# Kernel optimization log

Measured on AMD Instinct MI355X. Metric: run time of the kernel, lower is better.

Reference implementation:

```python
import jax, jax.numpy as jnp
import numpy as np

N = 50000
IN_DIM = 1024
HID = 64
HEADS = 4
OUT_DIM = 128
NEG_SLOPE = 0.2


def setup_inputs() -> dict:
    key = jax.random.key(0)
    ks = jax.random.split(key, 10)
    x = jax.random.normal(ks[0], (N, IN_DIM), dtype=jnp.float32)
    edge_index = jax.random.randint(ks[1], (2, 800000), 0, N, dtype=jnp.int64)
    # GATConv 1: input_dim -> hidden_dim, heads=HEADS, concat=True
    W1 = jax.random.normal(ks[2], (IN_DIM, HEADS * HID), dtype=jnp.float32) * (1.0 / np.sqrt(IN_DIM))
    att_src1 = jax.random.normal(ks[3], (HEADS, HID), dtype=jnp.float32) * 0.1
    att_dst1 = jax.random.normal(ks[4], (HEADS, HID), dtype=jnp.float32) * 0.1
    b1 = jnp.zeros((HEADS * HID,), dtype=jnp.float32)
    # GATConv 2: hidden_dim*heads -> output_dim, heads=1, concat=False
    W2 = jax.random.normal(ks[5], (HEADS * HID, OUT_DIM), dtype=jnp.float32) * (1.0 / np.sqrt(HEADS * HID))
    att_src2 = jax.random.normal(ks[6], (1, OUT_DIM), dtype=jnp.float32) * 0.1
    att_dst2 = jax.random.normal(ks[7], (1, OUT_DIM), dtype=jnp.float32) * 0.1
    b2 = jnp.zeros((OUT_DIM,), dtype=jnp.float32)
    return {"x": x, "edge_index": edge_index, "W1": W1, "att_src1": att_src1,
            "att_dst1": att_dst1, "b1": b1, "W2": W2, "att_src2": att_src2,
            "att_dst2": att_dst2, "b2": b2}


def _gat_conv(x, src, dst, W, a_src, a_dst, b, heads, concat):
    # x: [N, F_in]; src/dst: [E'] (self-loops already included)
    n = x.shape[0]
    h = (x @ W).reshape(n, heads, -1)                 # [N, H, D]
    # per-node attention halves (PyG style)
    alpha_s = jnp.sum(h * a_src[None], axis=-1)       # [N, H]
    alpha_d = jnp.sum(h * a_dst[None], axis=-1)       # [N, H]
    e = jax.nn.leaky_relu(alpha_s[src] + alpha_d[dst], NEG_SLOPE)  # [E', H]
    # segment softmax over incoming edges of each destination node
    m = jax.ops.segment_max(e, dst, num_segments=n)   # [N, H]
    m = jnp.where(jnp.isfinite(m), m, 0.0)
    e = jnp.exp(e - m[dst])
    s = jax.ops.segment_sum(e, dst, num_segments=n)   # [N, H]
    alpha = e / (s[dst] + 1e-16)                      # [E', H]
    out = jax.ops.segment_sum(h[src] * alpha[:, :, None], dst, num_segments=n)  # [N, H, D]
    out = out.reshape(n, -1) if concat else out.mean(axis=1)
    return out + b


def reference(x, edge_index, W1, att_src1, att_dst1, b1, W2, att_src2, att_dst2, b2):
    n = x.shape[0]
    # PyG GATConv default: add self-loops
    loops = jnp.arange(n, dtype=edge_index.dtype)
    src = jnp.concatenate([edge_index[0], loops])
    dst = jnp.concatenate([edge_index[1], loops])
    # dropout layers are identity in eval mode
    h = _gat_conv(x, src, dst, W1, att_src1, att_dst1, b1, HEADS, concat=True)
    h = jax.nn.elu(h)
    out = _gat_conv(h, src, dst, W2, att_src2, att_dst2, b2, 1, concat=False)
    # F.normalize(p=2, dim=-1)
    norm = jnp.maximum(jnp.linalg.norm(out, axis=-1, keepdims=True), 1e-12)
    return out / norm
```

## Files before the change

### kernel.cpp

```cpp
#include <hip/hip_runtime.h>
#include <math.h>

#define NNODES 50000
#define E0 800000
#define ETOT 850000
#define IN_DIM 1024
#define HEADS 4
#define C1 256
#define C2 128
#define NEG_SLOPE 0.2f

typedef short bf16x8 __attribute__((ext_vector_type(8)));
typedef float f32x4 __attribute__((ext_vector_type(4)));
typedef unsigned short ushort_t;

__device__ __forceinline__ void edge_sd(const int* __restrict__ ei, int e, int& s, int& d) {
    if (e < E0) { s = ei[e]; d = ei[E0 + e]; }
    else        { s = e - E0; d = s; }
}

__device__ __forceinline__ ushort_t f2b(float f) {
    unsigned u = __float_as_uint(f);
    return (ushort_t)((u + 0x7fffu + ((u >> 16) & 1u)) >> 16);
}
__device__ __forceinline__ float bf2f(ushort_t u) {
    return __uint_as_float((unsigned)u << 16);
}
__device__ __forceinline__ float lrelu(float v) { return v > 0.f ? v : NEG_SLOPE * v; }

__device__ __forceinline__ void gload_lds16(const void* g, void* l) {
    __builtin_amdgcn_global_load_lds(
        (const __attribute__((address_space(1))) unsigned int*)g,
        (__attribute__((address_space(3))) unsigned int*)l, 16, 0, 0);
}

__global__ __launch_bounds__(256) void wtrans_kernel(const float* __restrict__ W,
                                                     ushort_t* __restrict__ WT,
                                                     int K, int N)
{
    int idx = blockIdx.x * 256 + threadIdx.x;
    if (idx >= K * N) return;
    int k = idx / N, n = idx % N;
    WT[(size_t)n * K + k] = f2b(W[idx]);
}

__global__ __launch_bounds__(256, 3) void gemm_fb(const float* __restrict__ A,
                                                  const ushort_t* __restrict__ Bt,
                                                  ushort_t* __restrict__ Cb,
                                                  int M, int N, int K)
{
    __shared__ __align__(16) ushort_t As[2][4 * 128 * 8];
    __shared__ __align__(16) ushort_t Bs[2][4 * 128 * 8];

    const int tid  = threadIdx.x;
    const int lane = tid & 63;
    const int wid  = tid >> 6;
    const int wr   = wid >> 1, wc = wid & 1;
    const int rowBase = blockIdx.y * 128;
    const int colBase = blockIdx.x * 128;

    const int arow = tid >> 1;
    const int akh  = (tid & 1) * 2;
    const int aGRow = min(rowBase + arow, M - 1);
    const float* aptr = A + (size_t)aGRow * K + akh * 8;
    const int awoff0 = akh * 1024 + arow * 8;
    const int awoff1 = awoff0 + 1024;

    const ushort_t* bptr = Bt + (size_t)(colBase + lane) * K + wid * 8;
    const int bwoff0 = wid * 1024;
    const int bwoff1 = bwoff0 + 512;

    const int r0 = lane & 15;
    const int kh = lane >> 4;
    const int ardoff = kh * 1024 + (wr * 64 + r0) * 8;
    const int brdoff = kh * 1024 + (wc * 64 + r0) * 8;

    f32x4 zero = {0.f, 0.f, 0.f, 0.f};
    f32x4 acc[4][4];
    #pragma unroll
    for (int i = 0; i < 4; ++i)
        #pragma unroll
        for (int j = 0; j < 4; ++j) acc[i][j] = zero;

    {
        float4 f0 = *(const float4*)(aptr + 0);
        float4 f1 = *(const float4*)(aptr + 4);
        float4 f2 = *(const float4*)(aptr + 8);
        float4 f3 = *(const float4*)(aptr + 12);
        bf16x8 p0, p1;
        p0[0] = f2b(f0.x); p0[1] = f2b(f0.y); p0[2] = f2b(f0.z); p0[3] = f2b(f0.w);
        p0[4] = f2b(f1.x); p0[5] = f2b(f1.y); p0[6] = f2b(f1.z); p0[7] = f2b(f1.w);
        p1[0] = f2b(f2.x); p1[1] = f2b(f2.y); p1[2] = f2b(f2.z); p1[3] = f2b(f2.w);
        p1[4] = f2b(f3.x); p1[5] = f2b(f3.y); p1[6] = f2b(f3.z); p1[7] = f2b(f3.w);
        *(bf16x8*)&As[0][awoff0] = p0;
        *(bf16x8*)&As[0][awoff1] = p1;
        gload_lds16(bptr, &Bs[0][bwoff0]);
        gload_lds16(bptr + (size_t)64 * K, &Bs[0][bwoff1]);
    }
    __syncthreads();

    const ushort_t* rdA = As[0]; const ushort_t* rdB = Bs[0];
    ushort_t*       stA = As[1]; ushort_t*       stB = Bs[1];

    const int nt = K >> 5;
    for (int t = 0; t < nt; ++t) {
        const int kt = (t + 1) << 5;
        const bool has_next = kt < K;
        float4 f0, f1, f2, f3;
        if (has_next) {
            gload_lds16(bptr + kt, stB + bwoff0);
            gload_lds16(bptr + (size_t)64 * K + kt, stB + bwoff1);
            f0 = *(const float4*)(aptr + kt + 0);
            f1 = *(const float4*)(aptr + kt + 4);
            f2 = *(const float4*)(aptr + kt + 8);
            f3 = *(const float4*)(aptr + kt + 12);
        }

        bf16x8 af[4], bfr[4];
        #pragma unroll
        for (int fi = 0; fi < 4; ++fi) af[fi] = *(const bf16x8*)(rdA + ardoff + fi * 128);
        #pragma unroll
        for (int fj = 0; fj < 4; ++fj) bfr[fj] = *(const bf16x8*)(rdB + brdoff + fj * 128);
        #pragma unroll
        for (int fi = 0; fi < 4; ++fi)
            #pragma unroll
            for (int fj = 0; fj < 4; ++fj)
                acc[fi][fj] = __builtin_amdgcn_mfma_f32_16x16x32_bf16(
                    af[fi], bfr[fj], acc[fi][fj], 0, 0, 0);

        if (has_next) {
            bf16x8 p0, p1;
            p0[0] = f2b(f0.x); p0[1] = f2b(f0.y); p0[2] = f2b(f0.z); p0[3] = f2b(f0.w);
            p0[4] = f2b(f1.x); p0[5] = f2b(f1.y); p0[6] = f2b(f1.z); p0[7] = f2b(f1.w);
            p1[0] = f2b(f2.x); p1[1] = f2b(f2.y); p1[2] = f2b(f2.z); p1[3] = f2b(f2.w);
            p1[4] = f2b(f3.x); p1[5] = f2b(f3.y); p1[6] = f2b(f3.z); p1[7] = f2b(f3.w);
            *(bf16x8*)(stA + awoff0) = p0;
            *(bf16x8*)(stA + awoff1) = p1;
        }
        __syncthreads();
        const ushort_t* tA = rdA; rdA = stA; stA = (ushort_t*)tA;
        const ushort_t* tB = rdB; rdB = stB; stB = (ushort_t*)tB;
    }

    #pragma unroll
    for (int fi = 0; fi < 4; ++fi) {
        int row0 = rowBase + wr * 64 + fi * 16 + kh * 4;
        #pragma unroll
        for (int i = 0; i < 4; ++i) {
            int row = row0 + i;
            if (row < M) {
                #pragma unroll
                for (int fj = 0; fj < 4; ++fj)
                    Cb[(size_t)row * N + colBase + wc * 64 + fj * 16 + r0] = f2b(acc[fi][fj][i]);
            }
        }
    }
}

__global__ __launch_bounds__(256, 4) void gemm_bb(const ushort_t* __restrict__ Ab,
                                                  const ushort_t* __restrict__ Bt,
                                                  ushort_t* __restrict__ Cb,
                                                  int M, int N, int K)
{
    __shared__ __align__(16) ushort_t As[2][4 * 128 * 8];
    __shared__ __align__(16) ushort_t Bs[2][4 * 128 * 8];

    const int tid  = threadIdx.x;
    const int lane = tid & 63;
    const int wid  = tid >> 6;
    const int wr   = wid >> 1, wc = wid & 1;
    const int rowBase = blockIdx.y * 128;
    const int colBase = blockIdx.x * 128;

    const ushort_t* aptr0 = Ab + (size_t)min(rowBase + lane, M - 1) * K + wid * 8;
    const ushort_t* aptr1 = Ab + (size_t)min(rowBase + 64 + lane, M - 1) * K + wid * 8;
    const ushort_t* bptr  = Bt + (size_t)(colBase + lane) * K + wid * 8;
    const int woff0 = wid * 1024;
    const int woff1 = woff0 + 512;

    const int r0 = lane & 15;
    const int kh = lane >> 4;
    const int ardoff = kh * 1024 + (wr * 64 + r0) * 8;
    const int brdoff = kh * 1024 + (wc * 64 + r0) * 8;

    f32x4 zero = {0.f, 0.f, 0.f, 0.f};
    f32x4 acc[4][4];
    #pragma unroll
    for (int i = 0; i < 4; ++i)
        #pragma unroll
        for (int j = 0; j < 4; ++j) acc[i][j] = zero;

    gload_lds16(aptr0, &As[0][woff0]);
    gload_lds16(aptr1, &As[0][woff1]);
    gload_lds16(bptr,  &Bs[0][woff0]);
    gload_lds16(bptr + (size_t)64 * K, &Bs[0][woff1]);
    __syncthreads();

    const ushort_t* rdA = As[0]; const ushort_t* rdB = Bs[0];
    ushort_t*       stA = As[1]; ushort_t*       stB = Bs[1];

    const int nt = K >> 5;
    for (int t = 0; t < nt; ++t) {
        const int kt = (t + 1) << 5;
        if (kt < K) {
            gload_lds16(aptr0 + kt, stA + woff0);
            gload_lds16(aptr1 + kt, stA + woff1);
            gload_lds16(bptr + kt,  stB + woff0);
            gload_lds16(bptr + (size_t)64 * K + kt, stB + woff1);
        }

        bf16x8 af[4], bfr[4];
        #pragma unroll
        for (int fi = 0; fi < 4; ++fi) af[fi] = *(const bf16x8*)(rdA + ardoff + fi * 128);
        #pragma unroll
        for (int fj = 0; fj < 4; ++fj) bfr[fj] = *(const bf16x8*)(rdB + brdoff + fj * 128);
        #pragma unroll
        for (int fi = 0; fi < 4; ++fi)
            #pragma unroll
            for (int fj = 0; fj < 4; ++fj)
                acc[fi][fj] = __builtin_amdgcn_mfma_f32_16x16x32_bf16(
                    af[fi], bfr[fj], acc[fi][fj], 0, 0, 0);

        __syncthreads();
        const ushort_t* tA = rdA; rdA = stA; stA = (ushort_t*)tA;
        const ushort_t* tB = rdB; rdB = stB; stB = (ushort_t*)tB;
    }

    #pragma unroll
    for (int fi = 0; fi < 4; ++fi) {
        int row0 = rowBase + wr * 64 + fi * 16 + kh * 4;
        #pragma unroll
        for (int i = 0; i < 4; ++i) {
            int row = row0 + i;
            if (row < M) {
                #pragma unroll
                for (int fj = 0; fj < 4; ++fj)
                    Cb[(size_t)row * N + colBase + wc * 64 + fj * 16 + r0] = f2b(acc[fi][fj][i]);
            }
        }
    }
}

__global__ __launch_bounds__(256) void alpha1_kernel(const ushort_t* __restrict__ h1b,
                                                     const float* __restrict__ asrc,
                                                     const float* __restrict__ adst,
                                                     float* __restrict__ out_s,
                                                     float* __restrict__ out_d)
{
    int n = blockIdx.x;
    int t = threadIdx.x;
    float h = bf2f(h1b[(size_t)n * C1 + t]);
    float s = h * asrc[t];
    float d = h * adst[t];
    #pragma unroll
    for (int off = 32; off > 0; off >>= 1) {
        s += __shfl_down(s, off);
        d += __shfl_down(d, off);
    }
    if ((t & 63) == 0) {
        out_s[n * HEADS + (t >> 6)] = s;
        out_d[n * HEADS + (t >> 6)] = d;
    }
}

__global__ __launch_bounds__(64) void alpha2_kernel(const ushort_t* __restrict__ h2b,
                                                    const float* __restrict__ asrc,
                                                    const float* __restrict__ adst,
                                                    float* __restrict__ out_s,
                                                    float* __restrict__ out_d)
{
    int n = blockIdx.x;
    int t = threadIdx.x;
    float a = bf2f(h2b[(size_t)n * C2 + t]);
    float b = bf2f(h2b[(size_t)n * C2 + t + 64]);
    float s = a * asrc[t] + b * asrc[t + 64];
    float d = a * adst[t] + b * adst[t + 64];
    #pragma unroll
    for (int off = 32; off > 0; off >>= 1) {
        s += __shfl_down(s, off);
        d += __shfl_down(d, off);
    }
    if (t == 0) { out_s[n] = s; out_d[n] = d; }
}

__global__ __launch_bounds__(256) void deg_kernel(const int* __restrict__ ei,
                                                  int* __restrict__ deg)
{
    int e = blockIdx.x * blockDim.x + threadIdx.x;
    if (e >= ETOT) return;
    int s, d; edge_sd(ei, e, s, d);
    atomicAdd(&deg[d], 1);
}

#define SCAN_T 1024
__global__ __launch_bounds__(SCAN_T) void scan_kernel(const int* __restrict__ deg,
                                                      int* __restrict__ rowptr)
{
    __shared__ int wsum[16];
    __shared__ int chunk_tot;
    __shared__ int carry_s;
    const int t = threadIdx.x, lane = t & 63, w = t >> 6;
    if (t == 0) carry_s = 0;
    __syncthreads();
    for (int base = 0; base < NNODES; base += SCAN_T * 4) {
        int idx = base + t * 4;
        int v0 = (idx + 0 < NNODES) ? deg[idx + 0] : 0;
        int v1 = (idx + 1 < NNODES) ? deg[idx + 1] : 0;
        int v2 = (idx + 2 < NNODES) ? deg[idx + 2] : 0;
        int v3 = (idx + 3 < NNODES) ? deg[idx + 3] : 0;
        int p0 = v0, p1 = p0 + v1, p2 = p1 + v2, p3 = p2 + v3;
        int incl = p3;
        #pragma unroll
        for (int off = 1; off < 64; off <<= 1) {
            int nb = __shfl_up(incl, off);
            if (lane >= off) incl += nb;
        }
        if (lane == 63) wsum[w] = incl;
        __syncthreads();
        if (w == 0 && lane < 16) {
            int ws = wsum[lane];
            int wincl = ws;
            #pragma unroll
            for (int off = 1; off < 16; off <<= 1) {
                int nb = __shfl_up(wincl, off);
                if (lane >= off) wincl += nb;
            }
            wsum[lane] = wincl - ws;
            if (lane == 15) chunk_tot = wincl;
        }
        __syncthreads();
        int carry = carry_s;
        int basev = carry + wsum[w] + (incl - p3);
        if (idx + 0 < NNODES) rowptr[idx + 0] = basev;
        if (idx + 1 < NNODES) rowptr[idx + 1] = basev + p0;
        if (idx + 2 < NNODES) rowptr[idx + 2] = basev + p1;
        if (idx + 3 < NNODES) rowptr[idx + 3] = basev + p2;
        __syncthreads();
        if (t == 0) carry_s = carry + chunk_tot;
        __syncthreads();
    }
    if (threadIdx.x == 0) rowptr[NNODES] = carry_s;
}

__global__ __launch_bounds__(256) void scatter_kernel(const int* __restrict__ ei,
                                                      int* __restrict__ cursor,
                                                      int* __restrict__ srcs)
{
    int e = blockIdx.x * blockDim.x + threadIdx.x;
    if (e >= ETOT) return;
    int s, d; edge_sd(ei, e, s, d);
    int pos = atomicAdd(&cursor[d], 1);
    srcs[pos] = s;
}

__global__ __launch_bounds__(256) void weights1_kernel(const int* __restrict__ rowptr,
                                                       const int* __restrict__ srcs,
                                                       const float4* __restrict__ as1,
                                                       const float4* __restrict__ ad1,
                                                       float4* __restrict__ wbuf)
{
    int d = blockIdx.x * 4 + (threadIdx.x >> 6);
    if (d >= NNODES) return;
    int lane = threadIdx.x & 63;
    int beg = rowptr[d], end = rowptr[d + 1];
    float4 adv = ad1[d];
    float m0 = -INFINITY, m1 = -INFINITY, m2 = -INFINITY, m3 = -INFINITY;
    for (int i = beg + lane; i < end; i += 64) {
        int s = srcs[i];
        float4 av = as1[s];
        m0 = fmaxf(m0, lrelu(av.x + adv.x));
        m1 = fmaxf(m1, lrelu(av.y + adv.y));
        m2 = fmaxf(m2, lrelu(av.z + adv.z));
        m3 = fmaxf(m3, lrelu(av.w + adv.w));
    }
    #pragma unroll
    for (int off = 32; off > 0; off >>= 1) {
        m0 = fmaxf(m0, __shfl_xor(m0, off));
        m1 = fmaxf(m1, __shfl_xor(m1, off));
        m2 = fmaxf(m2, __shfl_xor(m2, off));
        m3 = fmaxf(m3, __shfl_xor(m3, off));
    }
    float s0 = 0.f, s1 = 0.f, s2 = 0.f, s3 = 0.f;
    for (int i = beg + lane; i < end; i += 64) {
        int s = srcs[i];
        float4 av = as1[s];
        float w0 = expf(lrelu(av.x + adv.x) - m0);
        float w1 = expf(lrelu(av.y + adv.y) - m1);
        float w2 = expf(lrelu(av.z + adv.z) - m2);
        float w3 = expf(lrelu(av.w + adv.w) - m3);
        wbuf[i] = make_float4(w0, w1, w2, w3);
        s0 += w0; s1 += w1; s2 += w2; s3 += w3;
    }
    #pragma unroll
    for (int off = 32; off > 0; off >>= 1) {
        s0 += __shfl_xor(s0, off);
        s1 += __shfl_xor(s1, off);
        s2 += __shfl_xor(s2, off);
        s3 += __shfl_xor(s3, off);
    }
    float i0 = 1.f / (s0 + 1e-16f), i1 = 1.f / (s1 + 1e-16f);
    float i2 = 1.f / (s2 + 1e-16f), i3 = 1.f / (s3 + 1e-16f);
    for (int i = beg + lane; i < end; i += 64) {
        float4 wv = wbuf[i];
        wbuf[i] = make_float4(wv.x * i0, wv.y * i1, wv.z * i2, wv.w * i3);
    }
}

__global__ __launch_bounds__(256) void weights2_kernel(const int* __restrict__ rowptr,
                                                       const int* __restrict__ srcs,
                                                       const float* __restrict__ as2,
                                                       const float* __restrict__ ad2,
                                                       float* __restrict__ wbuf)
{
    int d = blockIdx.x * 4 + (threadIdx.x >> 6);
    if (d >= NNODES) return;
    int lane = threadIdx.x & 63;
    int beg = rowptr[d], end = rowptr[d + 1];
    float adv = ad2[d];
    float m = -INFINITY;
    for (int i = beg + lane; i < end; i += 64)
        m = fmaxf(m, lrelu(as2[srcs[i]] + adv));
    #pragma unroll
    for (int off = 32; off > 0; off >>= 1) m = fmaxf(m, __shfl_xor(m, off));
    float sm = 0.f;
    for (int i = beg + lane; i < end; i += 64) {
        float w = expf(lrelu(as2[srcs[i]] + adv) - m);
        wbuf[i] = w;
        sm += w;
    }
    #pragma unroll
    for (int off = 32; off > 0; off >>= 1) sm += __shfl_xor(sm, off);
    float inv = 1.f / (sm + 1e-16f);
    for (int i = beg + lane; i < end; i += 64) wbuf[i] *= inv;
}

__global__ __launch_bounds__(256) void aggr1_csr(const int* __restrict__ rowptr,
                                                 const int* __restrict__ srcs,
                                                 const ushort_t* __restrict__ h1b,
                                                 const float* __restrict__ wbuf,
                                                 const float* __restrict__ b1,
                                                 ushort_t* __restrict__ out)
{
    int d = blockIdx.x;
    int t = threadIdx.x;
    int head = t >> 6;
    int beg = rowptr[d], end = rowptr[d + 1];
    float acc = 0.f;
    int i = beg;
    for (; i + 1 < end; i += 2) {
        int s0 = srcs[i], s1 = srcs[i + 1];
        float a0 = wbuf[i * 4 + head], a1 = wbuf[i * 4 + 4 + head];
        float v0 = bf2f(h1b[(size_t)s0 * C1 + t]);
        float v1 = bf2f(h1b[(size_t)s1 * C1 + t]);
        acc = fmaf(a0, v0, acc);
        acc = fmaf(a1, v1, acc);
    }
    if (i < end) {
        int s0 = srcs[i];
        acc = fmaf(wbuf[i * 4 + head], bf2f(h1b[(size_t)s0 * C1 + t]), acc);
    }
    float o = acc + b1[t];
    out[(size_t)d * C1 + t] = f2b(o > 0.f ? o : (expf(o) - 1.f));
}

__global__ __launch_bounds__(128) void aggr2_csr(const int* __restrict__ rowptr,
                                                 const int* __restrict__ srcs,
                                                 const ushort_t* __restrict__ h2b,
                                                 const float* __restrict__ wbuf,
                                                 const float* __restrict__ b2,
                                                 float* __restrict__ out)
{
    int d = blockIdx.x;
    int t = threadIdx.x;
    int beg = rowptr[d], end = rowptr[d + 1];
    float acc = 0.f;
    int i = beg;
    for (; i + 1 < end; i += 2) {
        int s0 = srcs[i], s1 = srcs[i + 1];
        float a0 = wbuf[i], a1 = wbuf[i + 1];
        float v0 = bf2f(h2b[(size_t)s0 * C2 + t]);
        float v1 = bf2f(h2b[(size_t)s1 * C2 + t]);
        acc = fmaf(a0, v0, acc);
        acc = fmaf(a1, v1, acc);
    }
    if (i < end) acc = fmaf(wbuf[i], bf2f(h2b[(size_t)srcs[i] * C2 + t]), acc);
    float o = acc + b2[t];
    __shared__ float red[2];
    float sq = o * o;
    #pragma unroll
    for (int off = 32; off > 0; off >>= 1) sq += __shfl_down(sq, off);
    if ((t & 63) == 0) red[t >> 6] = sq;
    __syncthreads();
    float total = red[0] + red[1];
    float inv = 1.0f / fmaxf(sqrtf(total), 1e-12f);
    out[(size_t)d * C2 + t] = o * inv;
}

extern "C" void kernel_launch(void* const* d_in, const int* in_sizes, int n_in,
                              void* d_out, int out_size, void* d_ws, size_t ws_size,
                              hipStream_t stream)
{
    const float* x     = (const float*)d_in[0];
    const int*   ei    = (const int*)d_in[1];
    const float* W1    = (const float*)d_in[2];
    const float* asrc1 = (const float*)d_in[3];
    const float* adst1 = (const float*)d_in[4];
    const float* b1    = (const float*)d_in[5];
    const float* W2    = (const float*)d_in[6];
    const float* asrc2 = (const float*)d_in[7];
    const float* adst2 = (const float*)d_in[8];
    const float* b2    = (const float*)d_in[9];
    float* out = (float*)d_out;

    char* ws = (char*)d_ws;
    size_t off = 0;
    auto alloc = [&](size_t nbytes) {
        void* p = ws + off;
        off += (nbytes + 15) & ~(size_t)15;
        return p;
    };
    ushort_t* h1b    = (ushort_t*)alloc((size_t)NNODES * C1 * 2);
    ushort_t* act1b  = (ushort_t*)alloc((size_t)NNODES * C1 * 2);
    ushort_t* h2b    = (ushort_t*)alloc((size_t)NNODES * C2 * 2);
    ushort_t* W1T    = (ushort_t*)alloc((size_t)C1 * IN_DIM * 2);
    ushort_t* W2T    = (ushort_t*)alloc((size_t)C2 * C1 * 2);
    float*    as1    = (float*)alloc((size_t)NNODES * HEADS * 4);
    float*    ad1    = (float*)alloc((size_t)NNODES * HEADS * 4);
    float*    as2    = (float*)alloc((size_t)NNODES * 4);
    float*    ad2    = (float*)alloc((size_t)NNODES * 4);
    float*    wbuf1  = (float*)alloc((size_t)ETOT * HEADS * 4);
    float*    wbuf2  = (float*)alloc((size_t)ETOT * 4);
    int*      deg    = (int*)alloc((size_t)NNODES * 4);
    int*      rowptr = (int*)alloc((size_t)(NNODES + 1) * 4);
    int*      cursor = (int*)alloc((size_t)(NNODES + 1) * 4);
    int*      srcs   = (int*)alloc((size_t)ETOT * 4);

    const int eb = (ETOT + 255) / 256;
    const int nb4 = (NNODES + 3) / 4;

    wtrans_kernel<<<(IN_DIM * C1 + 255) / 256, 256, 0, stream>>>(W1, W1T, IN_DIM, C1);
    wtrans_kernel<<<(C1 * C2 + 255) / 256, 256, 0, stream>>>(W2, W2T, C1, C2);

    hipMemsetAsync(deg, 0, (size_t)NNODES * 4, stream);
    deg_kernel<<<eb, 256, 0, stream>>>(ei, deg);
    scan_kernel<<<1, SCAN_T, 0, stream>>>(deg, rowptr);
    hipMemcpyAsync(cursor, rowptr, (size_t)(NNODES + 1) * 4, hipMemcpyDeviceToDevice, stream);
    scatter_kernel<<<eb, 256, 0, stream>>>(ei, cursor, srcs);

    dim3 g1(C1 / 128, (NNODES + 127) / 128);
    gemm_fb<<<g1, 256, 0, stream>>>(x, W1T, h1b, NNODES, C1, IN_DIM);
    alpha1_kernel<<<NNODES, 256, 0, stream>>>(h1b, asrc1, adst1, as1, ad1);
    weights1_kernel<<<nb4, 256, 0, stream>>>(rowptr, srcs, (const float4*)as1,
                                             (const float4*)ad1, (float4*)wbuf1);
    aggr1_csr<<<NNODES, 256, 0, stream>>>(rowptr, srcs, h1b, wbuf1, b1, act1b);

    dim3 g2(C2 / 128, (NNODES + 127) / 128);
    gemm_bb<<<g2, 256, 0, stream>>>(act1b, W2T, h2b, NNODES, C2, C1);
    alpha2_kernel<<<NNODES, 64, 0, stream>>>(h2b, asrc2, adst2, as2, ad2);
    weights2_kernel<<<nb4, 256, 0, stream>>>(rowptr, srcs, as2, ad2, wbuf2);
    aggr2_csr<<<NNODES, 128, 0, stream>>>(rowptr, srcs, h2b, wbuf2, b2, out);
}
```

Before: 539.5 us.

## Halve GEMM row tiles and aggregate one node per wavefront with vector loads

Both GEMMs change from 128x128 to 64x128 tiles, with a smaller A staging buffer and half the accumulators, and their occupancy hint rises to 6 blocks per CU. The aim is more blocks and more waves in flight for the tall-skinny GEMMs, at the cost of re-reading the B tile more often. The two aggregation kernels now give each node one 64-lane wavefront instead of a whole block, with vectorized bf16 gathers (4 or 2 channels per lane). The layer-2 L2 norm becomes a wave-level xor shuffle reduction, which removes the LDS exchange and __syncthreads.

```diff
diff --git a/kernel.cpp b/kernel.cpp
--- a/kernel.cpp
+++ b/kernel.cpp
@@ -44,27 +44,26 @@
     WT[(size_t)n * K + k] = f2b(W[idx]);
 }
 
-__global__ __launch_bounds__(256, 3) void gemm_fb(const float* __restrict__ A,
+__global__ __launch_bounds__(256, 6) void gemm_fb(const float* __restrict__ A,
                                                   const ushort_t* __restrict__ Bt,
                                                   ushort_t* __restrict__ Cb,
                                                   int M, int N, int K)
 {
-    __shared__ __align__(16) ushort_t As[2][4 * 128 * 8];
+    __shared__ __align__(16) ushort_t As[2][4 * 64 * 8];
     __shared__ __align__(16) ushort_t Bs[2][4 * 128 * 8];
 
     const int tid  = threadIdx.x;
     const int lane = tid & 63;
     const int wid  = tid >> 6;
     const int wr   = wid >> 1, wc = wid & 1;
-    const int rowBase = blockIdx.y * 128;
+    const int rowBase = blockIdx.y * 64;
     const int colBase = blockIdx.x * 128;
 
-    const int arow = tid >> 1;
-    const int akh  = (tid & 1) * 2;
+    const int arow = tid >> 2;
+    const int akc  = tid & 3;
     const int aGRow = min(rowBase + arow, M - 1);
-    const float* aptr = A + (size_t)aGRow * K + akh * 8;
-    const int awoff0 = akh * 1024 + arow * 8;
-    const int awoff1 = awoff0 + 1024;
+    const float* aptr = A + (size_t)aGRow * K + akc * 8;
+    const int awoff = akc * 512 + arow * 8;
 
     const ushort_t* bptr = Bt + (size_t)(colBase + lane) * K + wid * 8;
     const int bwoff0 = wid * 1024;
@@ -72,28 +71,23 @@
 
     const int r0 = lane & 15;
     const int kh = lane >> 4;
-    const int ardoff = kh * 1024 + (wr * 64 + r0) * 8;
+    const int ardoff = kh * 512 + (wr * 32 + r0) * 8;
     const int brdoff = kh * 1024 + (wc * 64 + r0) * 8;
 
     f32x4 zero = {0.f, 0.f, 0.f, 0.f};
-    f32x4 acc[4][4];
-    #pragma unroll
-    for (int i = 0; i < 4; ++i)
+    f32x4 acc[2][4];
+    #pragma unroll
+    for (int i = 0; i < 2; ++i)
         #pragma unroll
         for (int j = 0; j < 4; ++j) acc[i][j] = zero;
 
     {
         float4 f0 = *(const float4*)(aptr + 0);
         float4 f1 = *(const float4*)(aptr + 4);
-        float4 f2 = *(const float4*)(aptr + 8);
-        float4 f3 = *(const float4*)(aptr + 12);
-        bf16x8 p0, p1;
+        bf16x8 p0;
         p0[0] = f2b(f0.x); p0[1] = f2b(f0.y); p0[2] = f2b(f0.z); p0[3] = f2b(f0.w);
         p0[4] = f2b(f1.x); p0[5] = f2b(f1.y); p0[6] = f2b(f1.z); p0[7] = f2b(f1.w);
-        p1[0] = f2b(f2.x); p1[1] = f2b(f2.y); p1[2] = f2b(f2.z); p1[3] = f2b(f2.w);
-        p1[4] = f2b(f3.x); p1[5] = f2b(f3.y); p1[6] = f2b(f3.z); p1[7] = f2b(f3.w);
-        *(bf16x8*)&As[0][awoff0] = p0;
-        *(bf16x8*)&As[0][awoff1] = p1;
+        *(bf16x8*)&As[0][awoff] = p0;
         gload_lds16(bptr, &Bs[0][bwoff0]);
         gload_lds16(bptr + (size_t)64 * K, &Bs[0][bwoff1]);
     }
@@ -106,36 +100,31 @@
     for (int t = 0; t < nt; ++t) {
         const int kt = (t + 1) << 5;
         const bool has_next = kt < K;
-        float4 f0, f1, f2, f3;
+        float4 f0, f1;
         if (has_next) {
             gload_lds16(bptr + kt, stB + bwoff0);
             gload_lds16(bptr + (size_t)64 * K + kt, stB + bwoff1);
             f0 = *(const float4*)(aptr + kt + 0);
             f1 = *(const float4*)(aptr + kt + 4);
-            f2 = *(const float4*)(aptr + kt + 8);
-            f3 = *(const float4*)(aptr + kt + 12);
-        }
-
-        bf16x8 af[4], bfr[4];
-        #pragma unroll
-        for (int fi = 0; fi < 4; ++fi) af[fi] = *(const bf16x8*)(rdA + ardoff + fi * 128);
+        }
+
+        bf16x8 af[2], bfr[4];
+        #pragma unroll
+        for (int fi = 0; fi < 2; ++fi) af[fi] = *(const bf16x8*)(rdA + ardoff + fi * 128);
         #pragma unroll
         for (int fj = 0; fj < 4; ++fj) bfr[fj] = *(const bf16x8*)(rdB + brdoff + fj * 128);
         #pragma unroll
-        for (int fi = 0; fi < 4; ++fi)
+        for (int fi = 0; fi < 2; ++fi)
             #pragma unroll
             for (int fj = 0; fj < 4; ++fj)
                 acc[fi][fj] = __builtin_amdgcn_mfma_f32_16x16x32_bf16(
                     af[fi], bfr[fj], acc[fi][fj], 0, 0, 0);
 
         if (has_next) {
-            bf16x8 p0, p1;
+            bf16x8 p0;
             p0[0] = f2b(f0.x); p0[1] = f2b(f0.y); p0[2] = f2b(f0.z); p0[3] = f2b(f0.w);
             p0[4] = f2b(f1.x); p0[5] = f2b(f1.y); p0[6] = f2b(f1.z); p0[7] = f2b(f1.w);
-            p1[0] = f2b(f2.x); p1[1] = f2b(f2.y); p1[2] = f2b(f2.z); p1[3] = f2b(f2.w);
-            p1[4] = f2b(f3.x); p1[5] = f2b(f3.y); p1[6] = f2b(f3.z); p1[7] = f2b(f3.w);
-            *(bf16x8*)(stA + awoff0) = p0;
-            *(bf16x8*)(stA + awoff1) = p1;
+            *(bf16x8*)(stA + awoff) = p0;
         }
         __syncthreads();
         const ushort_t* tA = rdA; rdA = stA; stA = (ushort_t*)tA;
@@ -143,8 +132,8 @@
     }
 
     #pragma unroll
-    for (int fi = 0; fi < 4; ++fi) {
-        int row0 = rowBase + wr * 64 + fi * 16 + kh * 4;
+    for (int fi = 0; fi < 2; ++fi) {
+        int row0 = rowBase + wr * 32 + fi * 16 + kh * 4;
         #pragma unroll
         for (int i = 0; i < 4; ++i) {
             int row = row0 + i;
@@ -157,43 +146,42 @@
     }
 }
 
-__global__ __launch_bounds__(256, 4) void gemm_bb(const ushort_t* __restrict__ Ab,
+__global__ __launch_bounds__(256, 6) void gemm_bb(const ushort_t* __restrict__ Ab,
                                                   const ushort_t* __restrict__ Bt,
                                                   ushort_t* __restrict__ Cb,
                                                   int M, int N, int K)
 {
-    __shared__ __align__(16) ushort_t As[2][4 * 128 * 8];
+    __shared__ __align__(16) ushort_t As[2][4 * 64 * 8];
     __shared__ __align__(16) ushort_t Bs[2][4 * 128 * 8];
 
     const int tid  = threadIdx.x;
     const int lane = tid & 63;
     const int wid  = tid >> 6;
     const int wr   = wid >> 1, wc = wid & 1;
-    const int rowBase = blockIdx.y * 128;
+    const int rowBase = blockIdx.y * 64;
     const int colBase = blockIdx.x * 128;
 
-    const ushort_t* aptr0 = Ab + (size_t)min(rowBase + lane, M - 1) * K + wid * 8;
-    const ushort_t* aptr1 = Ab + (size_t)min(rowBase + 64 + lane, M - 1) * K + wid * 8;
-    const ushort_t* bptr  = Bt + (size_t)(colBase + lane) * K + wid * 8;
-    const int woff0 = wid * 1024;
-    const int woff1 = woff0 + 512;
+    const ushort_t* aptr = Ab + (size_t)min(rowBase + lane, M - 1) * K + wid * 8;
+    const ushort_t* bptr = Bt + (size_t)(colBase + lane) * K + wid * 8;
+    const int awoff  = wid * 512;
+    const int bwoff0 = wid * 1024;
+    const int bwoff1 = bwoff0 + 512;
 
     const int r0 = lane & 15;
     const int kh = lane >> 4;
-    const int ardoff = kh * 1024 + (wr * 64 + r0) * 8;
+    const int ardoff = kh * 512 + (wr * 32 + r0) * 8;
     const int brdoff = kh * 1024 + (wc * 64 + r0) * 8;
 
     f32x4 zero = {0.f, 0.f, 0.f, 0.f};
-    f32x4 acc[4][4];
-    #pragma unroll
-    for (int i = 0; i < 4; ++i)
+    f32x4 acc[2][4];
+    #pragma unroll
+    for (int i = 0; i < 2; ++i)
         #pragma unroll
         for (int j = 0; j < 4; ++j) acc[i][j] = zero;
 
-    gload_lds16(aptr0, &As[0][woff0]);
-    gload_lds16(aptr1, &As[0][woff1]);
-    gload_lds16(bptr,  &Bs[0][woff0]);
-    gload_lds16(bptr + (size_t)64 * K, &Bs[0][woff1]);
+    gload_lds16(aptr, &As[0][awoff]);
+    gload_lds16(bptr, &Bs[0][bwoff0]);
+    gload_lds16(bptr + (size_t)64 * K, &Bs[0][bwoff1]);
     __syncthreads();
 
     const ushort_t* rdA = As[0]; const ushort_t* rdB = Bs[0];
@@ -203,19 +191,18 @@
     for (int t = 0; t < nt; ++t) {
         const int kt = (t + 1) << 5;
         if (kt < K) {
-            gload_lds16(aptr0 + kt, stA + woff0);
-            gload_lds16(aptr1 + kt, stA + woff1);
-            gload_lds16(bptr + kt,  stB + woff0);
-            gload_lds16(bptr + (size_t)64 * K + kt, stB + woff1);
-        }
-
-        bf16x8 af[4], bfr[4];
-        #pragma unroll
-        for (int fi = 0; fi < 4; ++fi) af[fi] = *(const bf16x8*)(rdA + ardoff + fi * 128);
+            gload_lds16(aptr + kt, stA + awoff);
+            gload_lds16(bptr + kt, stB + bwoff0);
+            gload_lds16(bptr + (size_t)64 * K + kt, stB + bwoff1);
+        }
+
+        bf16x8 af[2], bfr[4];
+        #pragma unroll
+        for (int fi = 0; fi < 2; ++fi) af[fi] = *(const bf16x8*)(rdA + ardoff + fi * 128);
         #pragma unroll
         for (int fj = 0; fj < 4; ++fj) bfr[fj] = *(const bf16x8*)(rdB + brdoff + fj * 128);
         #pragma unroll
-        for (int fi = 0; fi < 4; ++fi)
+        for (int fi = 0; fi < 2; ++fi)
             #pragma unroll
             for (int fj = 0; fj < 4; ++fj)
                 acc[fi][fj] = __builtin_amdgcn_mfma_f32_16x16x32_bf16(
@@ -227,8 +214,8 @@
     }
 
     #pragma unroll
-    for (int fi = 0; fi < 4; ++fi) {
-        int row0 = rowBase + wr * 64 + fi * 16 + kh * 4;
+    for (int fi = 0; fi < 2; ++fi) {
+        int row0 = rowBase + wr * 32 + fi * 16 + kh * 4;
         #pragma unroll
         for (int i = 0; i < 4; ++i) {
             int row = row0 + i;
@@ -441,59 +428,76 @@
                                                  const float* __restrict__ b1,
                                                  ushort_t* __restrict__ out)
 {
-    int d = blockIdx.x;
-    int t = threadIdx.x;
-    int head = t >> 6;
+    int d = blockIdx.x * 4 + (threadIdx.x >> 6);
+    if (d >= NNODES) return;
+    int lane = threadIdx.x & 63;
+    int c0 = lane * 4;
+    int head = lane >> 4;
     int beg = rowptr[d], end = rowptr[d + 1];
-    float acc = 0.f;
+    float a0 = 0.f, a1 = 0.f, a2 = 0.f, a3 = 0.f;
     int i = beg;
     for (; i + 1 < end; i += 2) {
         int s0 = srcs[i], s1 = srcs[i + 1];
-        float a0 = wbuf[i * 4 + head], a1 = wbuf[i * 4 + 4 + head];
-        float v0 = bf2f(h1b[(size_t)s0 * C1 + t]);
-        float v1 = bf2f(h1b[(size_t)s1 * C1 + t]);
-        acc = fmaf(a0, v0, acc);
-        acc = fmaf(a1, v1, acc);
+        float w0 = wbuf[i * 4 + head], w1 = wbuf[i * 4 + 4 + head];
+        ushort4 v0 = *(const ushort4*)(h1b + (size_t)s0 * C1 + c0);
+        ushort4 v1 = *(const ushort4*)(h1b + (size_t)s1 * C1 + c0);
+        a0 = fmaf(w0, bf2f(v0.x), a0); a1 = fmaf(w0, bf2f(v0.y), a1);
+        a2 = fmaf(w0, bf2f(v0.z), a2); a3 = fmaf(w0, bf2f(v0.w), a3);
+        a0 = fmaf(w1, bf2f(v1.x), a0); a1 = fmaf(w1, bf2f(v1.y), a1);
+        a2 = fmaf(w1, bf2f(v1.z), a2); a3 = fmaf(w1, bf2f(v1.w), a3);
     }
     if (i < end) {
         int s0 = srcs[i];
-        acc = fmaf(wbuf[i * 4 + head], bf2f(h1b[(size_t)s0 * C1 + t]), acc);
-    }
-    float o = acc + b1[t];
-    out[(size_t)d * C1 + t] = f2b(o > 0.f ? o : (expf(o) - 1.f));
-}
-
-__global__ __launch_bounds__(128) void aggr2_csr(const int* __restrict__ rowptr,
+        float w0 = wbuf[i * 4 + head];
+        ushort4 v0 = *(const ushort4*)(h1b + (size_t)s0 * C1 + c0);
+        a0 = fmaf(w0, bf2f(v0.x), a0); a1 = fmaf(w0, bf2f(v0.y), a1);
+        a2 = fmaf(w0, bf2f(v0.z), a2); a3 = fmaf(w0, bf2f(v0.w), a3);
+    }
+    float4 bv = *(const float4*)(b1 + c0);
+    float o0 = a0 + bv.x, o1 = a1 + bv.y, o2 = a2 + bv.z, o3 = a3 + bv.w;
+    ushort4 r;
+    r.x = f2b(o0 > 0.f ? o0 : (expf(o0) - 1.f));
+    r.y = f2b(o1 > 0.f ? o1 : (expf(o1) - 1.f));
+    r.z = f2b(o2 > 0.f ? o2 : (expf(o2) - 1.f));
+    r.w = f2b(o3 > 0.f ? o3 : (expf(o3) - 1.f));
+    *(ushort4*)(out + (size_t)d * C1 + c0) = r;
+}
+
+__global__ __launch_bounds__(256) void aggr2_csr(const int* __restrict__ rowptr,
                                                  const int* __restrict__ srcs,
                                                  const ushort_t* __restrict__ h2b,
                                                  const float* __restrict__ wbuf,
                                                  const float* __restrict__ b2,
                                                  float* __restrict__ out)
 {
-    int d = blockIdx.x;
-    int t = threadIdx.x;
+    int d = blockIdx.x * 4 + (threadIdx.x >> 6);
+    if (d >= NNODES) return;
+    int lane = threadIdx.x & 63;
+    int c0 = lane * 2;
     int beg = rowptr[d], end = rowptr[d + 1];
-    float acc = 0.f;
+    float a0 = 0.f, a1 = 0.f;
     int i = beg;
     for (; i + 1 < end; i += 2) {
         int s0 = srcs[i], s1 = srcs[i + 1];
-        float a0 = wbuf[i], a1 = wbuf[i + 1];
-        float v0 = bf2f(h2b[(size_t)s0 * C2 + t]);
-        float v1 = bf2f(h2b[(size_t)s1 * C2 + t]);
-        acc = fmaf(a0, v0, acc);
-        acc = fmaf(a1, v1, acc);
-    }
-    if (i < end) acc = fmaf(wbuf[i], bf2f(h2b[(size_t)srcs[i] * C2 + t]), acc);
-    float o = acc + b2[t];
-    __shared__ float red[2];
-    float sq = o * o;
-    #pragma unroll
-    for (int off = 32; off > 0; off >>= 1) sq += __shfl_down(sq, off);
-    if ((t & 63) == 0) red[t >> 6] = sq;
-    __syncthreads();
-    float total = red[0] + red[1];
-    float inv = 1.0f / fmaxf(sqrtf(total), 1e-12f);
-    out[(size_t)d * C2 + t] = o * inv;
+        float w0 = wbuf[i], w1 = wbuf[i + 1];
+        ushort2 v0 = *(const ushort2*)(h2b + (size_t)s0 * C2 + c0);
+        ushort2 v1 = *(const ushort2*)(h2b + (size_t)s1 * C2 + c0);
+        a0 = fmaf(w0, bf2f(v0.x), a0); a1 = fmaf(w0, bf2f(v0.y), a1);
+        a0 = fmaf(w1, bf2f(v1.x), a0); a1 = fmaf(w1, bf2f(v1.y), a1);
+    }
+    if (i < end) {
+        float w0 = wbuf[i];
+        ushort2 v0 = *(const ushort2*)(h2b + (size_t)srcs[i] * C2 + c0);
+        a0 = fmaf(w0, bf2f(v0.x), a0); a1 = fmaf(w0, bf2f(v0.y), a1);
+    }
+    float2 bv = *(const float2*)(b2 + c0);
+    float o0 = a0 + bv.x, o1 = a1 + bv.y;
+    float sq = o0 * o0 + o1 * o1;
+    #pragma unroll
+    for (int off = 32; off > 0; off >>= 1) sq += __shfl_xor(sq, off);
+    float inv = 1.0f / fmaxf(sqrtf(sq), 1e-12f);
+    float2 r = make_float2(o0 * inv, o1 * inv);
+    *(float2*)(out + (size_t)d * C2 + c0) = r;
 }
 
 extern "C" void kernel_launch(void* const* d_in, const int* in_sizes, int n_in,
@@ -547,16 +551,16 @@
     hipMemcpyAsync(cursor, rowptr, (size_t)(NNODES + 1) * 4, hipMemcpyDeviceToDevice, stream);
     scatter_kernel<<<eb, 256, 0, stream>>>(ei, cursor, srcs);
 
-    dim3 g1(C1 / 128, (NNODES + 127) / 128);
+    dim3 g1(C1 / 128, (NNODES + 63) / 64);
     gemm_fb<<<g1, 256, 0, stream>>>(x, W1T, h1b, NNODES, C1, IN_DIM);
     alpha1_kernel<<<NNODES, 256, 0, stream>>>(h1b, asrc1, adst1, as1, ad1);
     weights1_kernel<<<nb4, 256, 0, stream>>>(rowptr, srcs, (const float4*)as1,
                                              (const float4*)ad1, (float4*)wbuf1);
-    aggr1_csr<<<NNODES, 256, 0, stream>>>(rowptr, srcs, h1b, wbuf1, b1, act1b);
-
-    dim3 g2(C2 / 128, (NNODES + 127) / 128);
+    aggr1_csr<<<nb4, 256, 0, stream>>>(rowptr, srcs, h1b, wbuf1, b1, act1b);
+
+    dim3 g2(C2 / 128, (NNODES + 63) / 64);
     gemm_bb<<<g2, 256, 0, stream>>>(act1b, W2T, h2b, NNODES, C2, C1);
     alpha2_kernel<<<NNODES, 64, 0, stream>>>(h2b, asrc2, adst2, as2, ad2);
     weights2_kernel<<<nb4, 256, 0, stream>>>(rowptr, srcs, as2, ad2, wbuf2);
-    aggr2_csr<<<NNODES, 128, 0, stream>>>(rowptr, srcs, h2b, wbuf2, b2, out);
-}
+    aggr2_csr<<<nb4, 256, 0, stream>>>(rowptr, srcs, h2b, wbuf2, b2, out);
+}
```

After: 489.6 us. 1.1x faster.
